# Kernel optimization log

Hardware: AMD Instinct MI355X
Metric: run time of the kernel (lower is better)

## Reference

```python
import jax, jax.numpy as jnp
import numpy as np
import math

B, S, V, D = 2, 2048, 32000, 256

def setup_inputs() -> dict:
    key = jax.random.key(0)
    ks = jax.random.split(key, 10)
    inp = jax.random.randint(ks[0], (B, S), 0, V)
    # causal mask, broadcast over batch
    mask = jnp.broadcast_to(jnp.tril(jnp.ones((S, S), dtype=bool)), (B, S, S))
    scale = 1.0 / math.sqrt(D)
    return {
        "input": inp,
        "mask": mask,
        "E": jax.random.normal(ks[1], (V, D), jnp.float32) * scale,
        "P": jax.random.normal(ks[2], (S, D), jnp.float32) * scale,
        "WQK1": jax.random.normal(ks[3], (D, D), jnp.float32) * scale,
        "WOV1": jax.random.normal(ks[4], (D, D), jnp.float32) * scale,
        "WQK2": jax.random.normal(ks[5], (D, D), jnp.float32) * scale,
        "WOV2": jax.random.normal(ks[6], (D, D), jnp.float32) * scale,
        "WF":   jax.random.normal(ks[7], (D, D), jnp.float32) * scale,
        "U":    jax.random.normal(ks[8], (V, D), jnp.float32) * scale,
    }

def _attn_block(X, WQK, WOV, mask, d_model):
    # S = (X @ WQK.T) @ X.T * sqrt(d)  -- note: MULTIPLY by sqrt(d), as in source
    scores = jnp.einsum('bsd,btd->bst', X @ WQK.T, X) * math.sqrt(d_model)
    scores = jnp.where(mask, scores, -jnp.inf)
    A = jax.nn.softmax(scores, axis=-1)  # dropout p=0 -> identity
    Y = jnp.einsum('bst,btd->bsd', A, X @ WOV.T)
    return X + Y

def reference(input, mask, E, P, WQK1, WOV1, WQK2, WOV2, WF, U):
    d_model = E.shape[1]
    X = E[input] + P[None, :, :]          # (B,S,D)
    X = _attn_block(X, WQK1, WOV1, mask, d_model)
    X = _attn_block(X, WQK2, WOV2, mask, d_model)
    X = X + X @ WF.T                      # FFN residual
    logits = X @ U.T                      # (B,S,V)
    return logits
```

## Files before the change

kernel.cpp:

```cpp
#include <hip/hip_runtime.h>
#include <math.h>

#define Bn 2
#define Sn 2048
#define Vn 32000
#define Dn 256
#define BSn (Bn * Sn)

typedef unsigned short u16;
typedef __attribute__((ext_vector_type(8))) __bf16 bf16x8;
typedef __attribute__((ext_vector_type(4))) float f32x4;
typedef __attribute__((ext_vector_type(8))) unsigned short u16x8;
typedef __attribute__((ext_vector_type(4))) unsigned short u16x4;

__device__ __forceinline__ u16 f2b(float v) {
    union { __bf16 b; u16 u; } c;
    c.b = (__bf16)v;
    return c.u;
}

#define GLOAD16(gp, lp)                                          \
    __builtin_amdgcn_global_load_lds(                            \
        (const __attribute__((address_space(1))) void*)(gp),     \
        (__attribute__((address_space(3))) void*)(lp), 16, 0, 0)

__device__ __forceinline__ float wred_max(float v) {
#pragma unroll
    for (int o = 32; o; o >>= 1) v = fmaxf(v, __shfl_xor(v, o, 64));
    return v;
}
__device__ __forceinline__ float wred_sum(float v) {
#pragma unroll
    for (int o = 32; o; o >>= 1) v += __shfl_xor(v, o, 64);
    return v;
}

__global__ __launch_bounds__(256) void k_prep(
    const int* __restrict__ inp, const float* __restrict__ E,
    const float* __restrict__ P, const float* __restrict__ WQK1,
    const float* __restrict__ WOV1, const float* __restrict__ WQK2,
    const float* __restrict__ WOV2, const float* __restrict__ WF,
    const float* __restrict__ U, float* __restrict__ Xf, u16* __restrict__ Xb,
    u16* __restrict__ Wqv1, u16* __restrict__ Wqv2, u16* __restrict__ Wfb,
    u16* __restrict__ Ub) {
    int bid = blockIdx.x;
    if (bid < 320) {
        int w = bid >> 6, blk = bid & 63;
        const float* src;
        u16* dst;
        switch (w) {
            case 0: src = WQK1; dst = Wqv1; break;
            case 1: src = WOV1; dst = Wqv1 + Dn * Dn; break;
            case 2: src = WQK2; dst = Wqv2; break;
            case 3: src = WOV2; dst = Wqv2 + Dn * Dn; break;
            default: src = WF; dst = Wfb; break;
        }
        int i = (blk * 256 + threadIdx.x) * 4;
        float4 v = *(const float4*)&src[i];
        u16x4 o;
        o.x = f2b(v.x); o.y = f2b(v.y); o.z = f2b(v.z); o.w = f2b(v.w);
        *(u16x4*)&dst[i] = o;
    } else if (bid < 8320) {
        int i = ((bid - 320) * 256 + threadIdx.x) * 4;
        float4 v = *(const float4*)&U[i];
        u16x4 o;
        o.x = f2b(v.x); o.y = f2b(v.y); o.z = f2b(v.z); o.w = f2b(v.w);
        *(u16x4*)&Ub[i] = o;
    } else {
        int bs = bid - 8320;
        int d = threadIdx.x;
        int tok = inp[bs];
        int s = bs & (Sn - 1);
        float v = E[(size_t)tok * Dn + d] + P[(size_t)s * Dn + d];
        Xf[(size_t)bs * Dn + d] = v;
        Xb[(size_t)bs * Dn + d] = f2b(v);
    }
}

template <bool HAS_RES, bool OUT_F32, bool OUT_BF16, bool CAUSAL_SKIP,
          bool QV_SPLIT, int CHUNK, int TN>
__global__ __launch_bounds__(256)
void k_mfma(const u16* __restrict__ A, const u16* __restrict__ Bb,
            const float* __restrict__ R, float* __restrict__ Cf,
            u16* __restrict__ Cb, u16* __restrict__ Ct, int M, int N, int K,
            int lda, int ldb, int ldc, float alpha, long long sA, long long sB,
            long long sC, long long sR, int ytiles) {
    int bx, by;
    if (CHUNK > 0) {
        int nwg = gridDim.x;
        int q = nwg >> 3;
        int bid = blockIdx.x;
        int wg = (bid & 7) * q + (bid >> 3);
        int per = CHUNK * ytiles;
        int ch = wg / per, rr = wg % per;
        bx = ch * CHUNK + rr % CHUNK;
        by = rr / CHUNK;
    } else {
        bx = blockIdx.x;
        by = blockIdx.y;
    }
    int bm0 = by * 128;
    int bn0 = bx * TN;
    if (CAUSAL_SKIP && bn0 > bm0 + 127) return;

    int zb = blockIdx.z;
    A += (long long)zb * sA;
    Bb += (long long)zb * sB;
    if (HAS_RES) R += (long long)zb * sR;
    if (OUT_F32) Cf += (long long)zb * sC;
    if (OUT_BF16) Cb += (long long)zb * sC;

    __shared__ alignas(16) u16 As[2][128 * 32];
    __shared__ alignas(16) u16 Bs[2][TN * 32];

    int tid = threadIdx.x;
    int lane = tid & 63;
    int wave = tid >> 6;

    constexpr int MF = (TN == 128) ? 4 : 2;
    int wr, wc;
    if (TN == 128) {
        wr = wave >> 1;
        wc = wave & 1;
    } else {
        wr = wave;
        wc = 0;
    }

    int fr = lane & 15;
    int kq = lane >> 4;
    int rq = kq * 4;

    f32x4 acc[MF][4] = {};

    int nt = K >> 5;

    auto STAGE = [&](int buf, int k0) {
#pragma unroll
        for (int c = 0; c < 2; ++c) {
            int idx = tid + c * 256;
            int r = idx >> 2, co = (idx & 3) << 3;
            GLOAD16(&A[(size_t)(bm0 + r) * lda + k0 + co], &As[buf][idx * 8]);
        }
#pragma unroll
        for (int c = 0; c < TN / 64; ++c) {
            int idx = tid + c * 256;
            int r = idx >> 2, co = (idx & 3) << 3;
            GLOAD16(&Bb[(size_t)(bn0 + r) * ldb + k0 + co], &Bs[buf][idx * 8]);
        }
    };

    STAGE(0, 0);
    __syncthreads();

    for (int t = 0; t < nt; ++t) {
        int cur = t & 1;
        if (t + 1 < nt) STAGE(cur ^ 1, (t + 1) << 5);

        bf16x8 a[MF], b[4];
#pragma unroll
        for (int m = 0; m < MF; ++m)
            a[m] = *(const bf16x8*)&As[cur]
                       [(wr * (MF * 16) + m * 16 + fr) * 32 + kq * 8];
#pragma unroll
        for (int n = 0; n < 4; ++n)
            b[n] = *(const bf16x8*)&Bs[cur]
                       [(wc * 64 + n * 16 + fr) * 32 + kq * 8];
#pragma unroll
        for (int m = 0; m < MF; ++m)
#pragma unroll
            for (int n = 0; n < 4; ++n)
                acc[m][n] = __builtin_amdgcn_mfma_f32_16x16x32_bf16(
                    a[m], b[n], acc[m][n], 0, 0, 0);
        __syncthreads();
    }

    if (QV_SPLIT && bn0 >= 256) {
#pragma unroll
        for (int m = 0; m < MF; ++m) {
#pragma unroll
            for (int n = 0; n < 4; ++n) {
                int gr = bm0 + wr * (MF * 16) + m * 16 + rq;
                int gc = bn0 + wc * 64 + n * 16 + fr - 256;
                int bb = gr / Sn;
                int ss = gr % Sn;
                u16x4 o;
#pragma unroll
                for (int i = 0; i < 4; ++i) o[i] = f2b(acc[m][n][i]);
                *(u16x4*)&Ct[((size_t)bb * Dn + gc) * Sn + ss] = o;
            }
        }
        return;
    }

#pragma unroll
    for (int m = 0; m < MF; ++m) {
#pragma unroll
        for (int n = 0; n < 4; ++n) {
            int gr = bm0 + wr * (MF * 16) + m * 16 + rq;
            int gc = bn0 + wc * 64 + n * 16 + fr;
#pragma unroll
            for (int i = 0; i < 4; ++i) {
                float v = acc[m][n][i] * alpha;
                size_t idx = (size_t)(gr + i) * ldc + gc;
                if (HAS_RES) v += R[idx];
                if (OUT_F32) Cf[idx] = v;
                if (OUT_BF16) Cb[idx] = f2b(v);
            }
        }
    }
}

__global__ __launch_bounds__(256)
void k_pv(const u16* __restrict__ Pb, const u16* __restrict__ Vt,
          const float* __restrict__ R, float* __restrict__ Cf,
          u16* __restrict__ Cb) {
    int bm0 = blockIdx.y * 64;
    int bn0 = blockIdx.x * 64;
    int zb = blockIdx.z;
    const u16* A = Pb + (long long)zb * Sn * Sn;
    const u16* Bb = Vt + (long long)zb * (long long)Dn * Sn;
    const float* Rz = R + (long long)zb * Sn * Dn;
    float* Cfz = Cf + (long long)zb * Sn * Dn;
    u16* Cbz = Cb + (long long)zb * Sn * Dn;

    __shared__ alignas(16) u16 As[3][64 * 32];
    __shared__ alignas(16) u16 Bs[3][64 * 32];

    int tid = threadIdx.x;
    int lane = tid & 63, wave = tid >> 6;
    int wr = wave >> 1, wc = wave & 1;
    int fr = lane & 15, kq = lane >> 4, rq = kq * 4;

    int nt = (bm0 + 64) >> 5;

    auto RSTAGE = [&](int buf, int t) {
        int k0 = t << 5;
        int r = tid >> 2, co = (tid & 3) << 3;
        GLOAD16(&A[(size_t)(bm0 + r) * Sn + k0 + co], &As[buf][tid * 8]);
        GLOAD16(&Bb[(size_t)(bn0 + r) * Sn + k0 + co], &Bs[buf][tid * 8]);
    };

    f32x4 acc[2][2] = {};
    RSTAGE(0, 0);
    RSTAGE(1, 1);

    for (int t = 0; t < nt; ++t) {
        if (t + 1 < nt)
            asm volatile("s_waitcnt vmcnt(2)" ::: "memory");
        else
            asm volatile("s_waitcnt vmcnt(0)" ::: "memory");
        __builtin_amdgcn_s_barrier();
        __builtin_amdgcn_sched_barrier(0);
        if (t + 2 < nt) RSTAGE((t + 2) % 3, t + 2);

        int cur = t % 3;
        bf16x8 a[2], b[2];
#pragma unroll
        for (int m = 0; m < 2; ++m)
            a[m] = *(const bf16x8*)&As[cur]
                       [(wr * 32 + m * 16 + fr) * 32 + kq * 8];
#pragma unroll
        for (int n = 0; n < 2; ++n)
            b[n] = *(const bf16x8*)&Bs[cur]
                       [(wc * 32 + n * 16 + fr) * 32 + kq * 8];
#pragma unroll
        for (int m = 0; m < 2; ++m)
#pragma unroll
            for (int n = 0; n < 2; ++n)
                acc[m][n] = __builtin_amdgcn_mfma_f32_16x16x32_bf16(
                    a[m], b[n], acc[m][n], 0, 0, 0);
    }

#pragma unroll
    for (int m = 0; m < 2; ++m) {
#pragma unroll
        for (int n = 0; n < 2; ++n) {
            int gr = bm0 + wr * 32 + m * 16 + rq;
            int gc = bn0 + wc * 32 + n * 16 + fr;
#pragma unroll
            for (int i = 0; i < 4; ++i) {
                float v = acc[m][n][i];
                size_t idx = (size_t)(gr + i) * Dn + gc;
                v += Rz[idx];
                Cfz[idx] = v;
                Cbz[idx] = f2b(v);
            }
        }
    }
}

__global__ __launch_bounds__(256) void k_softmax(const float* __restrict__ Sc,
                                                 u16* __restrict__ Pb) {
    int bs = blockIdx.x;
    int b = bs >> 11, s = bs & 2047;
    const float* row = Sc + ((size_t)b << 22) + ((size_t)s << 11);
    u16* prow = Pb + ((size_t)b << 22) + ((size_t)s << 11);
    int tid = threadIdx.x;
    int n = s + 1;
    int nc = (n + 127) & ~127;

    float v[8];
#pragma unroll
    for (int j = 0; j < 8; ++j) {
        int t = tid + j * 256;
        v[j] = (t < n) ? row[t] : -INFINITY;
    }

    float m = v[0];
#pragma unroll
    for (int j = 1; j < 8; ++j) m = fmaxf(m, v[j]);
    m = wred_max(m);

    __shared__ float red[8];
    int lane = tid & 63, w = tid >> 6;
    if (lane == 0) red[w] = m;
    __syncthreads();
    m = fmaxf(fmaxf(red[0], red[1]), fmaxf(red[2], red[3]));

    float sum = 0.0f;
#pragma unroll
    for (int j = 0; j < 8; ++j) {
        v[j] = __expf(v[j] - m);
        sum += v[j];
    }
    sum = wred_sum(sum);
    if (lane == 0) red[4 + w] = sum;
    __syncthreads();
    float inv = 1.0f / (red[4] + red[5] + red[6] + red[7]);

#pragma unroll
    for (int j = 0; j < 8; ++j) {
        int t = tid + j * 256;
        if (t < nc) prow[t] = f2b(v[j] * inv);
    }
}

static void launch_layer(const float* XfIn, float* XfOut, u16* Xb,
                         const u16* Wqv, u16* Qb, u16* Vt, float* Sc, u16* Pb,
                         hipStream_t stream) {
    k_mfma<false, false, true, false, true, 0, 64>
        <<<dim3(8, 32, 1), 256, 0, stream>>>(
            Xb, Wqv, nullptr, nullptr, Qb, Vt, BSn, 512, Dn, Dn, Dn, Dn, 1.0f,
            0, 0, 0, 0, 0);
    k_mfma<false, true, false, true, false, 0, 128>
        <<<dim3(Sn / 128, Sn / 128, Bn), 256, 0, stream>>>(
            Qb, Xb, nullptr, Sc, nullptr, nullptr, Sn, Sn, Dn, Dn, Dn, Sn,
            16.0f, (long long)Sn * Dn, (long long)Sn * Dn, (long long)Sn * Sn,
            0, 0);
    k_softmax<<<Bn * Sn, 256, 0, stream>>>(Sc, Pb);
    k_pv<<<dim3(Dn / 64, Sn / 64, Bn), 256, 0, stream>>>(Pb, Vt, XfIn, XfOut,
                                                         Xb);
}

extern "C" void kernel_launch(void* const* d_in, const int* in_sizes, int n_in,
                              void* d_out, int out_size, void* d_ws,
                              size_t ws_size, hipStream_t stream) {
    const int* inp = (const int*)d_in[0];
    const float* E = (const float*)d_in[2];
    const float* P = (const float*)d_in[3];
    const float* WQK1 = (const float*)d_in[4];
    const float* WOV1 = (const float*)d_in[5];
    const float* WQK2 = (const float*)d_in[6];
    const float* WOV2 = (const float*)d_in[7];
    const float* WF = (const float*)d_in[8];
    const float* U = (const float*)d_in[9];
    float* out = (float*)d_out;

    char* p = (char*)d_ws;
    auto alloc = [&](size_t bytes) {
        void* r = (void*)p;
        p += (bytes + 255) & ~(size_t)255;
        return r;
    };

    float* XfA = (float*)alloc((size_t)BSn * Dn * 4);
    float* XfB = (float*)alloc((size_t)BSn * Dn * 4);
    float* Sc = (float*)alloc((size_t)Bn * Sn * Sn * 4);
    u16* Xb = (u16*)alloc((size_t)BSn * Dn * 2);
    u16* Qb = (u16*)alloc((size_t)BSn * Dn * 2);
    u16* Vt = (u16*)alloc((size_t)Bn * Dn * Sn * 2);
    u16* Fb = (u16*)alloc((size_t)BSn * Dn * 2);
    u16* Pb = (u16*)alloc((size_t)Bn * Sn * Sn * 2);
    u16* Wqv1 = (u16*)alloc((size_t)512 * Dn * 2);
    u16* Wqv2 = (u16*)alloc((size_t)512 * Dn * 2);
    u16* Wfb = (u16*)alloc((size_t)Dn * Dn * 2);
    u16* Ub = (u16*)alloc((size_t)Vn * Dn * 2);

    k_prep<<<12416, 256, 0, stream>>>(inp, E, P, WQK1, WOV1, WQK2, WOV2, WF, U,
                                      XfA, Xb, Wqv1, Wqv2, Wfb, Ub);

    launch_layer(XfA, XfB, Xb, Wqv1, Qb, Vt, Sc, Pb, stream);
    launch_layer(XfB, XfA, Xb, Wqv2, Qb, Vt, Sc, Pb, stream);

    k_mfma<true, false, true, false, false, 0, 64>
        <<<dim3(4, 32, 1), 256, 0, stream>>>(
            Xb, Wfb, XfA, nullptr, Fb, nullptr, BSn, Dn, Dn, Dn, Dn, Dn, 1.0f,
            0, 0, 0, 0, 0);

    k_mfma<false, true, false, false, false, 25, 128>
        <<<dim3((Vn / 128) * (BSn / 128), 1, 1), 256, 0, stream>>>(
            Fb, Ub, nullptr, out, nullptr, nullptr, BSn, Vn, Dn, Dn, Dn, Vn,
            1.0f, 0, 0, 0, 0, BSn / 128);
}
```

Baseline: 262.8 us.

## Deepen PV load pipeline, vectorize softmax I/O, shrink score GEMM tile

The PV kernel's LDS ring grows from 3 to 6 stages, so five tiles are in flight instead of two, with vmcnt waits sized to the number of tiles still outstanding. The softmax kernel now reads rows as float4 and writes bf16 in groups of four, cutting memory instruction count. The score GEMM switches to a 64-wide N tile template, doubling the number of blocks in x. The deeper ring roughly doubles LDS use in the PV kernel and may lower occupancy, and the smaller score tile reduces data reuse per block.

```diff
diff --git a/kernel.cpp b/kernel.cpp
--- a/kernel.cpp
+++ b/kernel.cpp
@@ -224,8 +224,8 @@
     float* Cfz = Cf + (long long)zb * Sn * Dn;
     u16* Cbz = Cb + (long long)zb * Sn * Dn;
 
-    __shared__ alignas(16) u16 As[3][64 * 32];
-    __shared__ alignas(16) u16 Bs[3][64 * 32];
+    __shared__ alignas(16) u16 As[6][64 * 32];
+    __shared__ alignas(16) u16 Bs[6][64 * 32];
 
     int tid = threadIdx.x;
     int lane = tid & 63, wave = tid >> 6;
@@ -242,19 +242,27 @@
     };
 
     f32x4 acc[2][2] = {};
-    RSTAGE(0, 0);
-    RSTAGE(1, 1);
+#pragma unroll
+    for (int s = 0; s < 5; ++s)
+        if (s < nt) RSTAGE(s, s);
 
     for (int t = 0; t < nt; ++t) {
-        if (t + 1 < nt)
+        int rem = nt - 1 - t;
+        if (rem >= 4)
+            asm volatile("s_waitcnt vmcnt(8)" ::: "memory");
+        else if (rem == 3)
+            asm volatile("s_waitcnt vmcnt(6)" ::: "memory");
+        else if (rem == 2)
+            asm volatile("s_waitcnt vmcnt(4)" ::: "memory");
+        else if (rem == 1)
             asm volatile("s_waitcnt vmcnt(2)" ::: "memory");
         else
             asm volatile("s_waitcnt vmcnt(0)" ::: "memory");
         __builtin_amdgcn_s_barrier();
         __builtin_amdgcn_sched_barrier(0);
-        if (t + 2 < nt) RSTAGE((t + 2) % 3, t + 2);
-
-        int cur = t % 3;
+        if (t + 5 < nt) RSTAGE((t + 5) % 6, t + 5);
+
+        int cur = t % 6;
         bf16x8 a[2], b[2];
 #pragma unroll
         for (int m = 0; m < 2; ++m)
@@ -295,6 +303,7 @@
     int bs = blockIdx.x;
     int b = bs >> 11, s = bs & 2047;
     const float* row = Sc + ((size_t)b << 22) + ((size_t)s << 11);
+    const float4* row4 = (const float4*)row;
     u16* prow = Pb + ((size_t)b << 22) + ((size_t)s << 11);
     int tid = threadIdx.x;
     int n = s + 1;
@@ -302,9 +311,13 @@
 
     float v[8];
 #pragma unroll
-    for (int j = 0; j < 8; ++j) {
-        int t = tid + j * 256;
-        v[j] = (t < n) ? row[t] : -INFINITY;
+    for (int j = 0; j < 2; ++j) {
+        float4 q = row4[tid + j * 256];
+        int e0 = (tid + j * 256) * 4;
+        v[j * 4 + 0] = (e0 + 0 < n) ? q.x : -INFINITY;
+        v[j * 4 + 1] = (e0 + 1 < n) ? q.y : -INFINITY;
+        v[j * 4 + 2] = (e0 + 2 < n) ? q.z : -INFINITY;
+        v[j * 4 + 3] = (e0 + 3 < n) ? q.w : -INFINITY;
     }
 
     float m = v[0];
@@ -330,9 +343,16 @@
     float inv = 1.0f / (red[4] + red[5] + red[6] + red[7]);
 
 #pragma unroll
-    for (int j = 0; j < 8; ++j) {
-        int t = tid + j * 256;
-        if (t < nc) prow[t] = f2b(v[j] * inv);
+    for (int j = 0; j < 2; ++j) {
+        int e0 = (tid + j * 256) * 4;
+        if (e0 < nc) {
+            u16x4 o;
+            o[0] = f2b(v[j * 4 + 0] * inv);
+            o[1] = f2b(v[j * 4 + 1] * inv);
+            o[2] = f2b(v[j * 4 + 2] * inv);
+            o[3] = f2b(v[j * 4 + 3] * inv);
+            *(u16x4*)&prow[e0] = o;
+        }
     }
 }
 
@@ -343,8 +363,8 @@
         <<<dim3(8, 32, 1), 256, 0, stream>>>(
             Xb, Wqv, nullptr, nullptr, Qb, Vt, BSn, 512, Dn, Dn, Dn, Dn, 1.0f,
             0, 0, 0, 0, 0);
-    k_mfma<false, true, false, true, false, 0, 128>
-        <<<dim3(Sn / 128, Sn / 128, Bn), 256, 0, stream>>>(
+    k_mfma<false, true, false, true, false, 0, 64>
+        <<<dim3(Sn / 64, Sn / 128, Bn), 256, 0, stream>>>(
             Qb, Xb, nullptr, Sc, nullptr, nullptr, Sn, Sn, Dn, Dn, Dn, Sn,
             16.0f, (long long)Sn * Dn, (long long)Sn * Dn, (long long)Sn * Sn,
             0, 0);
```

After: 262.5 us, median of 2. About the same (-0.1%).
